# Kernel tuning notes

Hardware: AMD Instinct MI355X
Metric: run time of the kernel (lower is better)

Reference implementation:

```python
import jax, jax.numpy as jnp
import numpy as np


def setup_inputs() -> dict:
    key = jax.random.key(0)
    kx, kw = jax.random.split(key)
    # x: [batch, seq, in_features]
    x = jax.random.normal(kx, (4, 2048, 4096), dtype=jnp.float32)
    # packed uint8-style weight: [(out_features+3)//4, in_features] = [4096, 4096]
    weight = jax.random.randint(kw, (4096, 4096), 0, 256, dtype=jnp.int32)
    return {"x": x, "weight": weight}


def reference(x, weight):
    # Faithful to BitLinear.forward: cast packed weight to x.dtype, then F.linear
    # (no unpacking, no weight_scale applied, bias disabled -> omitted).
    w = weight.astype(x.dtype)  # [packed_out, in]
    # y[b,s,o] = sum_d x[b,s,d] * w[o,d]
    y = jnp.einsum("bsd,od->bso", x, w)
    return y
```

## Files before the change

### kernel.cpp

```cpp
#include <hip/hip_runtime.h>


typedef __bf16 bf16x8 __attribute__((ext_vector_type(8)));
typedef float f32x4 __attribute__((ext_vector_type(4)));
typedef unsigned short u16;
typedef u16 u16x8 __attribute__((ext_vector_type(8)));

__device__ __forceinline__ u16 f2bf(float f) {
    unsigned int u = __builtin_bit_cast(unsigned int, f);
    u = (u + 0x7FFFu + ((u >> 16) & 1u)) >> 16;
    return (u16)u;
}

__global__ void cvt_fused_k(const float* __restrict__ x, const int* __restrict__ w,
                            u16* __restrict__ xb, u16* __restrict__ wb,
                            int nxv, int nwv) {
    const int stride = gridDim.x * blockDim.x;
    for (int i = blockIdx.x * blockDim.x + threadIdx.x; i < nxv + nwv; i += stride) {
        if (i < nxv) {
            const float4* p = (const float4*)x;
            float4 a = p[2 * (size_t)i];
            float4 b = p[2 * (size_t)i + 1];
            u16x8 o;
            o[0] = f2bf(a.x); o[1] = f2bf(a.y); o[2] = f2bf(a.z); o[3] = f2bf(a.w);
            o[4] = f2bf(b.x); o[5] = f2bf(b.y); o[6] = f2bf(b.z); o[7] = f2bf(b.w);
            *(u16x8*)(xb + 8 * (size_t)i) = o;
        } else {
            int j = i - nxv;
            const int4* p = (const int4*)w;
            int4 a = p[2 * (size_t)j];
            int4 b = p[2 * (size_t)j + 1];
            u16x8 o;
            o[0] = f2bf((float)a.x); o[1] = f2bf((float)a.y); o[2] = f2bf((float)a.z); o[3] = f2bf((float)a.w);
            o[4] = f2bf((float)b.x); o[5] = f2bf((float)b.y); o[6] = f2bf((float)b.z); o[7] = f2bf((float)b.w);
            *(u16x8*)(wb + 8 * (size_t)j) = o;
        }
    }
}


#define STAGE(SBUF, SMAT, SKH, SKT)                                            \
    {                                                                          \
        const u16* gb = ((SMAT) == 0) ? Ab : Bb;                               \
        _Pragma("unroll")                                                      \
        for (int j = 0; j < 2; ++j) {                                          \
            const int c = wid * 2 + j;                                         \
            const u16* src = gb + (size_t)(c * 16 + srow) * K                  \
                             + (SKT) + (SKH) * 32 + ssig;                      \
            __builtin_amdgcn_global_load_lds(                                  \
                (const __attribute__((address_space(1))) void*)src,            \
                (__attribute__((address_space(3))) void*)(                     \
                    lds + (((SBUF) * 2 + (SMAT)) * 2 + (SKH)) * 8192 + c * 512), \
                16, 0, 0);                                                     \
        }                                                                      \
    }

#define PHASE(PBUF, CH, KH, SBUF, SMAT, SKH, SKT, DOVM)                        \
    {                                                                          \
        if ((CH) == 0) {                                                       \
            _Pragma("unroll")                                                  \
            for (int n = 0; n < 4; ++n)                                        \
                bfrag[n] = *(const bf16x8*)((const char*)lds                   \
                    + (((PBUF) * 2 + 1) * 2 + (KH)) * 16384                    \
                    + (wc * 64 + n * 16 + fr) * 64 + rd_sl);                   \
        }                                                                      \
        bf16x8 afrag[4];                                                       \
        _Pragma("unroll")                                                      \
        for (int mi = 0; mi < 4; ++mi)                                         \
            afrag[mi] = *(const bf16x8*)((const char*)lds                      \
                + (((PBUF) * 2 + 0) * 2 + (KH)) * 16384                        \
                + (wr * 128 + ((CH) * 4 + mi) * 16 + fr) * 64 + rd_sl);        \
        STAGE(SBUF, SMAT, SKH, SKT);                                           \
        if (DOVM) asm volatile("s_waitcnt vmcnt(4)" ::: "memory");             \
        asm volatile("s_barrier" ::: "memory");                                \
        __builtin_amdgcn_s_setprio(1);                                         \
        _Pragma("unroll")                                                      \
        for (int mi = 0; mi < 4; ++mi)                                         \
            _Pragma("unroll")                                                  \
            for (int n = 0; n < 4; ++n)                                        \
                acc[(CH) * 4 + mi][n] = __builtin_amdgcn_mfma_f32_16x16x32_bf16( \
                    afrag[mi], bfrag[n], acc[(CH) * 4 + mi][n], 0, 0, 0);      \
        __builtin_amdgcn_s_setprio(0);                                         \
        asm volatile("s_barrier" ::: "memory");                                \
    }

__global__ __launch_bounds__(512, 2)
void gemm_bf16_8ph(const u16* __restrict__ A, const u16* __restrict__ B,
                   float* __restrict__ C, int M, int N, int K) {
    __shared__ u16 lds[65536];

    const int tid  = threadIdx.x;
    const int lane = tid & 63;
    const int wid  = tid >> 6;
    const int wr   = wid >> 2;
    const int wc   = wid & 3;
    const int fr   = lane & 15;
    const int g    = lane >> 4;

    const int nwg = gridDim.x;
    const int cpx = nwg >> 3;
    const int bid = blockIdx.x;
    const int swz = (bid & 7) * cpx + (bid >> 3);
    const int tiles_n = N / 256;
    const int row0 = (swz / tiles_n) * 256;
    const int col0 = (swz % tiles_n) * 256;

    const int srow = lane >> 2;
    const int ssig = (((lane & 3) ^ ((lane >> 2) & 3))) * 8;

    const u16* Ab = A + (size_t)row0 * K;
    const u16* Bb = B + (size_t)col0 * K;

    const int rd_sl = (g ^ (fr & 3)) << 4;

    f32x4 acc[8][4] = {};
    bf16x8 bfrag[4];

    STAGE(0, 0, 0, 0);
    STAGE(0, 1, 0, 0);
    STAGE(0, 0, 1, 0);
    STAGE(0, 1, 1, 0);
    STAGE(1, 0, 0, 64);
    STAGE(1, 1, 0, 64);
    asm volatile("s_waitcnt vmcnt(4)" ::: "memory");
    asm volatile("s_barrier" ::: "memory");

    const int KMASK = K - 1;
    int kt = 0;
    for (int i = 0; i < K / 128; ++i) {
        const int k2 = (kt + 128) & KMASK;
        const int k3 = (kt + 192) & KMASK;
        PHASE(0, 0, 0,  1, 0, 1, kt + 64, false);
        PHASE(0, 1, 0,  1, 1, 1, kt + 64, false);
        PHASE(0, 0, 1,  0, 0, 0, k2,      false);
        PHASE(0, 1, 1,  0, 1, 0, k2,      true);
        PHASE(1, 0, 0,  0, 0, 1, k2,      false);
        PHASE(1, 1, 0,  0, 1, 1, k2,      false);
        PHASE(1, 0, 1,  1, 0, 0, k3,      false);
        PHASE(1, 1, 1,  1, 1, 0, k3,      true);
        kt += 128;
    }

    const int crow0 = row0 + wr * 128 + g * 4;
    const int ccol0 = col0 + wc * 64 + fr;
#pragma unroll
    for (int mf = 0; mf < 8; ++mf) {
#pragma unroll
        for (int n = 0; n < 4; ++n) {
            const size_t base = (size_t)(crow0 + mf * 16) * N + ccol0 + n * 16;
#pragma unroll
            for (int r = 0; r < 4; ++r)
                C[base + (size_t)r * N] = acc[mf][n][r];
        }
    }
}

extern "C" void kernel_launch(void* const* d_in, const int* in_sizes, int n_in,
                              void* d_out, int out_size, void* d_ws, size_t ws_size,
                              hipStream_t stream) {
    const float* x = (const float*)d_in[0];
    const int*   w = (const int*)d_in[1];
    float*     out = (float*)d_out;

    const int M = 8192, N = 4096, K = 4096;

    u16* xb = (u16*)d_ws;
    u16* wb = xb + (size_t)M * K;

    {
        int nxv = (M * K) / 8;
        int nwv = (N * K) / 8;
        cvt_fused_k<<<dim3(4096), dim3(256), 0, stream>>>(x, w, xb, wb, nxv, nwv);
    }

    dim3 grid((M / 256) * (N / 256));
    gemm_bf16_8ph<<<grid, dim3(512), 0, stream>>>(xb, wb, out, M, N, K);
}
```

Before: 509.9 us.

## Split conversion kernels with nontemporal loads and change LDS swizzle pattern

The fused grid-stride conversion kernel becomes two separate kernels, one for x and one for the weight. Each uses a flat grid with two vectors per thread and nontemporal loads, which removes the per-iteration branch and the loop overhead. The LDS XOR swizzle for the GEMM is also changed so the write pattern uses lane bits 3-4 and the read pattern uses fr>>1. This is meant to reduce LDS bank conflicts on the MFMA fragment reads. The swizzle change is only correct if the reads and writes still map consistently to each other.

```diff
diff --git a/kernel.cpp b/kernel.cpp
--- a/kernel.cpp
+++ b/kernel.cpp
@@ -5,36 +5,46 @@
 typedef float f32x4 __attribute__((ext_vector_type(4)));
 typedef unsigned short u16;
 typedef u16 u16x8 __attribute__((ext_vector_type(8)));
+typedef unsigned int u32x4 __attribute__((ext_vector_type(4)));
 
-__device__ __forceinline__ u16 f2bf(float f) {
-    unsigned int u = __builtin_bit_cast(unsigned int, f);
-    u = (u + 0x7FFFu + ((u >> 16) & 1u)) >> 16;
-    return (u16)u;
+__device__ __forceinline__ u16 f2bf_bits(unsigned int u) {
+    return (u16)((u + 0x7FFFu + ((u >> 16) & 1u)) >> 16);
+}
+__device__ __forceinline__ u16 i2bf(int v) {
+    return f2bf_bits(__builtin_bit_cast(unsigned int, (float)v));
 }
 
-__global__ void cvt_fused_k(const float* __restrict__ x, const int* __restrict__ w,
-                            u16* __restrict__ xb, u16* __restrict__ wb,
-                            int nxv, int nwv) {
-    const int stride = gridDim.x * blockDim.x;
-    for (int i = blockIdx.x * blockDim.x + threadIdx.x; i < nxv + nwv; i += stride) {
-        if (i < nxv) {
-            const float4* p = (const float4*)x;
-            float4 a = p[2 * (size_t)i];
-            float4 b = p[2 * (size_t)i + 1];
-            u16x8 o;
-            o[0] = f2bf(a.x); o[1] = f2bf(a.y); o[2] = f2bf(a.z); o[3] = f2bf(a.w);
-            o[4] = f2bf(b.x); o[5] = f2bf(b.y); o[6] = f2bf(b.z); o[7] = f2bf(b.w);
-            *(u16x8*)(xb + 8 * (size_t)i) = o;
-        } else {
-            int j = i - nxv;
-            const int4* p = (const int4*)w;
-            int4 a = p[2 * (size_t)j];
-            int4 b = p[2 * (size_t)j + 1];
-            u16x8 o;
-            o[0] = f2bf((float)a.x); o[1] = f2bf((float)a.y); o[2] = f2bf((float)a.z); o[3] = f2bf((float)a.w);
-            o[4] = f2bf((float)b.x); o[5] = f2bf((float)b.y); o[6] = f2bf((float)b.z); o[7] = f2bf((float)b.w);
-            *(u16x8*)(wb + 8 * (size_t)j) = o;
-        }
+__global__ void cvt_x_k(const float* __restrict__ x, u16* __restrict__ xb) {
+    const size_t t = (size_t)blockIdx.x * blockDim.x + threadIdx.x;
+    const u32x4* p = (const u32x4*)x;
+#pragma unroll
+    for (int v = 0; v < 2; ++v) {
+        const size_t i = 2 * t + v;
+        u32x4 a = __builtin_nontemporal_load(&p[2 * i]);
+        u32x4 b = __builtin_nontemporal_load(&p[2 * i + 1]);
+        u16x8 o;
+        o[0] = f2bf_bits(a[0]); o[1] = f2bf_bits(a[1]);
+        o[2] = f2bf_bits(a[2]); o[3] = f2bf_bits(a[3]);
+        o[4] = f2bf_bits(b[0]); o[5] = f2bf_bits(b[1]);
+        o[6] = f2bf_bits(b[2]); o[7] = f2bf_bits(b[3]);
+        *(u16x8*)(xb + 8 * i) = o;
+    }
+}
+
+__global__ void cvt_w_k(const int* __restrict__ w, u16* __restrict__ wb) {
+    const size_t t = (size_t)blockIdx.x * blockDim.x + threadIdx.x;
+    const u32x4* p = (const u32x4*)w;
+#pragma unroll
+    for (int v = 0; v < 2; ++v) {
+        const size_t i = 2 * t + v;
+        u32x4 a = __builtin_nontemporal_load(&p[2 * i]);
+        u32x4 b = __builtin_nontemporal_load(&p[2 * i + 1]);
+        u16x8 o;
+        o[0] = i2bf((int)a[0]); o[1] = i2bf((int)a[1]);
+        o[2] = i2bf((int)a[2]); o[3] = i2bf((int)a[3]);
+        o[4] = i2bf((int)b[0]); o[5] = i2bf((int)b[1]);
+        o[6] = i2bf((int)b[2]); o[7] = i2bf((int)b[3]);
+        *(u16x8*)(wb + 8 * i) = o;
     }
 }
 
@@ -106,12 +116,12 @@
     const int col0 = (swz % tiles_n) * 256;
 
     const int srow = lane >> 2;
-    const int ssig = (((lane & 3) ^ ((lane >> 2) & 3))) * 8;
+    const int ssig = ((lane & 3) ^ ((lane >> 3) & 3)) * 8;
 
     const u16* Ab = A + (size_t)row0 * K;
     const u16* Bb = B + (size_t)col0 * K;
 
-    const int rd_sl = (g ^ (fr & 3)) << 4;
+    const int rd_sl = (g ^ ((fr >> 1) & 3)) << 4;
 
     f32x4 acc[8][4] = {};
     bf16x8 bfrag[4];
@@ -167,11 +177,8 @@
     u16* xb = (u16*)d_ws;
     u16* wb = xb + (size_t)M * K;
 
-    {
-        int nxv = (M * K) / 8;
-        int nwv = (N * K) / 8;
-        cvt_fused_k<<<dim3(4096), dim3(256), 0, stream>>>(x, w, xb, wb, nxv, nwv);
-    }
+    cvt_x_k<<<dim3(8192), dim3(256), 0, stream>>>(x, xb);
+    cvt_w_k<<<dim3(4096), dim3(256), 0, stream>>>(w, wb);
 
     dim3 grid((M / 256) * (N / 256));
     gemm_bf16_8ph<<<grid, dim3(512), 0, stream>>>(xb, wb, out, M, N, K);
```

New measurement: 483.5 us. -5.2%, faster.
